# Performance work log

Measured on AMD Instinct MI355X. Metric: run time of the kernel, lower is better.

The kernel has to match this reference:

```python
import jax, jax.numpy as jnp
import numpy as np

D_MODEL = 1024
NUM_HEADS = 16
HEAD_DIM = D_MODEL // NUM_HEADS


def setup_inputs() -> dict:
    key = jax.random.key(0)
    ks = jax.random.split(key, 11)
    B, S, D = 2, 2048, D_MODEL
    scale = 1.0 / np.sqrt(D)
    inp = {
        "q": jax.random.normal(ks[0], (B, S, D), dtype=jnp.float32),
        "k": jax.random.normal(ks[1], (B, S, D), dtype=jnp.float32),
        "v": jax.random.normal(ks[2], (B, S, D), dtype=jnp.float32),
        # torch nn.Linear weights are [out, in]; y = x @ W.T + b
        "Wq": jax.random.normal(ks[3], (D, D), dtype=jnp.float32) * scale,
        "bq": jnp.zeros((D,), dtype=jnp.float32),
        "Wk": jax.random.normal(ks[4], (D, D), dtype=jnp.float32) * scale,
        "bk": jnp.zeros((D,), dtype=jnp.float32),
        "Wv": jax.random.normal(ks[5], (D, D), dtype=jnp.float32) * scale,
        "bv": jnp.zeros((D,), dtype=jnp.float32),
        "Wo": jax.random.normal(ks[6], (D, D), dtype=jnp.float32) * scale,
        "bo": jnp.zeros((D,), dtype=jnp.float32),
    }
    return inp


def _split_heads(x):
    B, S, D = x.shape
    return x.reshape(B, S, NUM_HEADS, HEAD_DIM).transpose(0, 2, 1, 3)  # [B,H,S,hd]


def reference(q, k, v, Wq, bq, Wk, bk, Wv, bv, Wo, bo):
    B, S, D = q.shape
    qh = _split_heads(q @ Wq.T + bq)
    kh = _split_heads(k @ Wk.T + bk)
    vh = _split_heads(v @ Wv.T + bv)
    # scores: [B,H,S,S], causal mask, softmax
    scores = jnp.einsum("bhqd,bhkd->bhqk", qh, kh) / jnp.sqrt(
        jnp.asarray(HEAD_DIM, dtype=qh.dtype))
    causal = jnp.tril(jnp.ones((S, S), dtype=bool))
    scores = jnp.where(causal[None, None], scores, -jnp.inf)
    attn = jax.nn.softmax(scores, axis=-1)
    out = jnp.einsum("bhqk,bhkd->bhqd", attn, vh)  # [B,H,S,hd]
    out = out.transpose(0, 2, 1, 3).reshape(B, S, D)
    return out @ Wo.T + bo
```

## Files before the change

kernel.cpp:

```cpp
#include <hip/hip_runtime.h>
#include <hip/hip_bf16.h>
#include <cstdint>
#include <cstddef>

typedef __bf16 bf16;
typedef __bf16 bf16x2 __attribute__((ext_vector_type(2)));
typedef __bf16 bf16x4 __attribute__((ext_vector_type(4)));
typedef __bf16 bf16x8 __attribute__((ext_vector_type(8)));
typedef float f32x4 __attribute__((ext_vector_type(4)));
typedef float f32x16 __attribute__((ext_vector_type(16)));
typedef unsigned int u32x4 __attribute__((ext_vector_type(4)));

#define S_LEN 2048
#define DM 1024
#define NH 16
#define HD 64
#define NQKV (4096 * 1024)
#define NW (1024 * 1024)
#define QK_SCALE 0.18033688011112042f

__device__ __forceinline__ void gload_lds16(const bf16* g, bf16* l) {
  __builtin_amdgcn_global_load_lds(
      (const __attribute__((address_space(1))) void*)g,
      (__attribute__((address_space(3))) void*)l, 16, 0, 0);
}

__device__ __forceinline__ unsigned packbf(float lo, float hi) {
  bf16x2 t;
  t[0] = (bf16)lo;
  t[1] = (bf16)hi;
  return __builtin_bit_cast(unsigned, t);
}

__device__ __forceinline__ void pl32swap(unsigned& a, unsigned& b) {
#if __has_builtin(__builtin_amdgcn_permlane32_swap)
  auto r = __builtin_amdgcn_permlane32_swap((int)a, (int)b, false, false);
  a = (unsigned)r[0];
  b = (unsigned)r[1];
#else
  asm volatile("v_permlane32_swap_b32 %0, %1" : "+v"(a), "+v"(b));
#endif
}

__global__ __launch_bounds__(256) void cvt_all(
    const float* __restrict__ q, const float* __restrict__ k, const float* __restrict__ v,
    const float* __restrict__ Wq, const float* __restrict__ Wk, const float* __restrict__ Wv,
    const float* __restrict__ Wo, bf16* __restrict__ out) {
  const size_t i = ((size_t)blockIdx.x * 256 + threadIdx.x) * 8;
  const float* src;
  size_t off;
  if (i < (size_t)NQKV) { src = q; off = i; }
  else if (i < 2ull * NQKV) { src = k; off = i - NQKV; }
  else if (i < 3ull * NQKV) { src = v; off = i - 2ull * NQKV; }
  else {
    const size_t j = i - 3ull * NQKV;
    if (j < (size_t)NW) { src = Wq; off = j; }
    else if (j < 2ull * NW) { src = Wk; off = j - NW; }
    else if (j < 3ull * NW) { src = Wv; off = j - 2ull * NW; }
    else { src = Wo; off = j - 3ull * NW; }
  }
  const float4 a = *(const float4*)(src + off);
  const float4 b = *(const float4*)(src + off + 4);
  bf16x8 o;
  o[0] = (bf16)a.x; o[1] = (bf16)a.y; o[2] = (bf16)a.z; o[3] = (bf16)a.w;
  o[4] = (bf16)b.x; o[5] = (bf16)b.y; o[6] = (bf16)b.z; o[7] = (bf16)b.w;
  *(bf16x8*)(out + i) = o;
}

template <int MODE>
__global__ __launch_bounds__(256, 2) void gemm_bt(
    const bf16* __restrict__ A, const bf16* __restrict__ W,
    const float* __restrict__ bias0, const float* __restrict__ bias1,
    const float* __restrict__ bias2, void* __restrict__ Out,
    int M, int N, int K, float scale) {
  __shared__ __align__(16) bf16 sm[2 * 128 * 64];
  bf16* Asl = sm;
  bf16* Bsl = sm + 128 * 64;
  const int tid = threadIdx.x;
  const int lane = tid & 63, w = tid >> 6;
  const int wr = w >> 1, wc = w & 1;
  const int r16 = lane & 15, grp = lane >> 4;

  int flat = blockIdx.y * gridDim.x + blockIdx.x;
  const int cpx = (gridDim.x * gridDim.y) >> 3;
  flat = (flat & 7) * cpx + (flat >> 3);
  const int m0 = (flat / gridDim.x) * 128;
  const int n0 = (flat % gridDim.x) * 128;

  const int seg = n0 >> 10;
  const bf16* Ab = (MODE == 3) ? A + (size_t)seg * NQKV : A;

  f32x4 acc[4][4] = {};

  const int nk = K >> 6;
  for (int t = 0; t < nk; ++t) {
    const int k0 = t << 6;
    __syncthreads();
#pragma unroll
    for (int j = 0; j < 4; ++j) {
      const int lin = j * 256 + tid;
      const int rr = lin >> 3;
      const int cc = (lin & 7) * 8;
      gload_lds16(&Ab[(size_t)(m0 + rr) * K + k0 + cc], &Asl[lin * 8]);
      gload_lds16(&W[(size_t)(n0 + rr) * K + k0 + cc], &Bsl[lin * 8]);
    }
    __syncthreads();
#pragma unroll
    for (int kk = 0; kk < 2; ++kk) {
      bf16x8 af[4], bfr[4];
#pragma unroll
      for (int m = 0; m < 4; ++m)
        af[m] = *(const bf16x8*)&Asl[(wr * 64 + m * 16 + r16) * 64 + kk * 32 + grp * 8];
#pragma unroll
      for (int n = 0; n < 4; ++n)
        bfr[n] = *(const bf16x8*)&Bsl[(wc * 64 + n * 16 + r16) * 64 + kk * 32 + grp * 8];
#pragma unroll
      for (int m = 0; m < 4; ++m)
#pragma unroll
        for (int n = 0; n < 4; ++n)
          acc[m][n] = __builtin_amdgcn_mfma_f32_16x16x32_bf16(af[m], bfr[n], acc[m][n], 0, 0, 0);
    }
  }

  const float* bp = (MODE == 3) ? (seg == 0 ? bias0 : (seg == 1 ? bias1 : bias2)) : bias0;
  const float sc = (MODE == 3) ? (seg == 0 ? scale : 1.0f) : scale;

  if (MODE == 3 && seg == 2) {
    __syncthreads();
    bf16* T = sm + w * (32 * 76);
    const int b = (m0 + wr * 64) >> 11;
    const int srow0 = (m0 + wr * 64) & 2047;
    bf16* base2 = (bf16*)Out + 2 * (size_t)NQKV;
#pragma unroll
    for (int p = 0; p < 2; ++p) {
#pragma unroll
      for (int nn = 0; nn < 2; ++nn) {
        const int n = 2 * p + nn;
#pragma unroll
        for (int mq = 0; mq < 4; ++mq)
#pragma unroll
          for (int r = 0; r < 4; ++r) {
            const int d_l = nn * 16 + r16;
            const int s_l = mq * 16 + grp * 4 + r;
            const int cs = (n0 + wc * 64 + n * 16 + r16) & 1023;
            T[d_l * 76 + s_l] = (bf16)(acc[mq][n][r] + bp[cs]);
          }
      }
      __syncthreads();
#pragma unroll
      for (int j = 0; j < 4; ++j) {
        const int d_l = j * 8 + (lane >> 3);
        const int scnk = lane & 7;
        const uint2 lo = *(const uint2*)&T[d_l * 76 + scnk * 8];
        const uint2 hi = *(const uint2*)&T[d_l * 76 + scnk * 8 + 4];
        const int cs = (n0 + wc * 64 + p * 32 + d_l) & 1023;
        const int hh = cs >> 6, dd = cs & 63;
        bf16* dst = base2 + ((size_t)(b * NH + hh) * HD + dd) * S_LEN + srow0 + scnk * 8;
        uint4 val; val.x = lo.x; val.y = lo.y; val.z = hi.x; val.w = hi.y;
        *(uint4*)dst = val;
      }
      __syncthreads();
    }
    return;
  }

#pragma unroll
  for (int m = 0; m < 4; ++m) {
#pragma unroll
    for (int n = 0; n < 4; ++n) {
#pragma unroll
      for (int r = 0; r < 4; ++r) {
        const int row = m0 + wr * 64 + m * 16 + grp * 4 + r;
        const int col = n0 + wc * 64 + n * 16 + r16;
        const int cs = col & 1023;
        const float v = (acc[m][n][r] + bp[cs]) * sc;
        if (MODE == 3) {
          const int b = row >> 11, s = row & 2047, h = cs >> 6, d = cs & 63;
          bf16* base = (bf16*)Out + (size_t)seg * NQKV;
          base[((size_t)(b * NH + h) * S_LEN + s) * HD + d] = (bf16)v;
        } else {
          ((float*)Out)[(size_t)row * N + col] = v;
        }
      }
    }
  }
}

__global__ __launch_bounds__(256, 2) void attn_fwd6(
    const bf16* __restrict__ Qh, const bf16* __restrict__ Kh,
    const bf16* __restrict__ Vt, bf16* __restrict__ AO) {
  __shared__ __align__(16) bf16 Kl[3][64 * 64];
  __shared__ __align__(16) bf16 Vl[3][64 * 64];

  const int tid = threadIdx.x;
  const int lane = tid & 63, w = tid >> 6;
  const int q31 = lane & 31, h = lane >> 5;

  const int bid = blockIdx.x;
  const int xcd = bid & 7;
  const int within = bid >> 3;
  const int bh = xcd * 4 + (within >> 4);
  const int cc = (within < 32) ? 15 - (within & 15) : (within & 15);
  const int q0 = cc * 128;
  const int nt = 2 * cc + 2;
  const int q0w = q0 + 32 * w;
  const int nt_w = (q0w >> 6) + 1;
  const int qg = q0w + q31;

  const bf16* Qb = Qh + (size_t)bh * S_LEN * HD;
  const bf16* Kb = Kh + (size_t)bh * S_LEN * HD;
  const bf16* Vb = Vt + (size_t)bh * HD * S_LEN;

  int stK[2], stV[2], stL[2];
#pragma unroll
  for (int i = 0; i < 2; ++i) {
    const int lin = i * 256 + tid;
    const int row = lin >> 3;
    const int colb = (lin & 7) * 16;
    const int scol = colb ^ ((row & 7) << 4);
    stK[i] = row * HD + (scol >> 1);
    stV[i] = row * S_LEN + (scol >> 1);
    stL[i] = lin * 8;
  }

  bf16x8 qf[4];
#pragma unroll
  for (int ks = 0; ks < 4; ++ks)
    qf[ks] = *(const bf16x8*)&Qb[(size_t)qg * HD + ks * 16 + 8 * h];

  f32x16 accO[2] = {};
  float m = -1e30f, l = 0.f;
  const int swz = (q31 & 7) << 4;

#pragma unroll
  for (int i = 0; i < 2; ++i) {
    gload_lds16(&Kb[stK[i]], &Kl[0][stL[i]]);
    gload_lds16(&Vb[stV[i]], &Vl[0][stL[i]]);
  }
  if (nt > 1) {
#pragma unroll
    for (int i = 0; i < 2; ++i) {
      gload_lds16(&Kb[(size_t)64 * HD + stK[i]], &Kl[1][stL[i]]);
      gload_lds16(&Vb[64 + stV[i]], &Vl[1][stL[i]]);
    }
  }

  int cur = 0;
  for (int kt = 0; kt < nt; ++kt) {
    if (kt + 1 < nt) asm volatile("s_waitcnt vmcnt(4)" ::: "memory");
    else             asm volatile("s_waitcnt vmcnt(0)" ::: "memory");
    __builtin_amdgcn_s_barrier();

    if (kt + 2 < nt) {
      int nxt = cur + 2; if (nxt >= 3) nxt -= 3;
      const int kn = (kt + 2) << 6;
      bf16* kd = Kl[nxt];
      bf16* vd = Vl[nxt];
#pragma unroll
      for (int i = 0; i < 2; ++i) {
        gload_lds16(&Kb[(size_t)kn * HD + stK[i]], &kd[stL[i]]);
        gload_lds16(&Vb[kn + stV[i]], &vd[stL[i]]);
      }
    }

    if (kt < nt_w) {
      const int k0 = kt << 6;
      const bf16* KlC = Kl[cur];
      const bf16* VlC = Vl[cur];
      const bool diag = (kt == nt_w - 1);
      const bool skip1 = diag && (k0 + 32 > q0w + 31);

      bf16x8 kf[8];
#pragma unroll
      for (int ks = 0; ks < 4; ++ks) {
        const int c = (32 * ks + 16 * h) ^ swz;
        kf[ks] = *(const bf16x8*)((const char*)KlC + q31 * 128 + c);
      }
      if (!skip1) {
#pragma unroll
        for (int ks = 0; ks < 4; ++ks) {
          const int c = (32 * ks + 16 * h) ^ swz;
          kf[4 + ks] = *(const bf16x8*)((const char*)KlC + (32 + q31) * 128 + c);
        }
      }

      f32x16 p0 = {}, p1 = {};
      __builtin_amdgcn_s_setprio(1);
#pragma unroll
      for (int ks = 0; ks < 4; ++ks)
        p0 = __builtin_amdgcn_mfma_f32_32x32x16_bf16(kf[ks], qf[ks], p0, 0, 0, 0);
      __builtin_amdgcn_s_setprio(0);
      if (!skip1) {
        __builtin_amdgcn_s_setprio(1);
#pragma unroll
        for (int ks = 0; ks < 4; ++ks)
          p1 = __builtin_amdgcn_mfma_f32_32x32x16_bf16(kf[4 + ks], qf[ks], p1, 0, 0, 0);
        __builtin_amdgcn_s_setprio(0);
      } else {
#pragma unroll
        for (int r = 0; r < 16; ++r) p1[r] = -1e30f;
      }

      bf16x8 vf01[4];
#pragma unroll
      for (int ks = 0; ks < 2; ++ks)
#pragma unroll
        for (int db = 0; db < 2; ++db) {
          const int c = (32 * ks + 16 * h) ^ swz;
          vf01[ks * 2 + db] =
              *(const bf16x8*)((const char*)VlC + (db * 32 + q31) * 128 + c);
        }

      if (diag) {
#pragma unroll
        for (int r = 0; r < 16; ++r) {
          const int key = k0 + (r & 3) + 8 * (r >> 2) + 4 * h;
          if (key > qg) p0[r] = -1e30f;
          if (!skip1 && key + 32 > qg) p1[r] = -1e30f;
        }
      }
      float t[16];
#pragma unroll
      for (int r = 0; r < 16; ++r) t[r] = fmaxf(p0[r], p1[r]);
#pragma unroll
      for (int s = 8; s >= 1; s >>= 1)
#pragma unroll
        for (int r = 0; r < s; ++r) t[r] = fmaxf(t[r], t[r + s]);
      const float pmax = fmaxf(t[0], __shfl_xor(t[0], 32));
      if (!__all(pmax - m <= 8.0f)) {
        const float mn = fmaxf(m, pmax);
        const float alpha = exp2f(m - mn);
        m = mn;
        l *= alpha;
#pragma unroll
        for (int r = 0; r < 16; ++r) { accO[0][r] *= alpha; accO[1][r] *= alpha; }
      }
      float smv[16];
#pragma unroll
      for (int r = 0; r < 16; ++r) {
        p0[r] = exp2f(p0[r] - m);
        p1[r] = exp2f(p1[r] - m);
        smv[r] = p0[r] + p1[r];
      }
#pragma unroll
      for (int s = 8; s >= 1; s >>= 1)
#pragma unroll
        for (int r = 0; r < s; ++r) smv[r] += smv[r + s];
      l += smv[0] + __shfl_xor(smv[0], 32);

      unsigned pw[4][4];
#define PACK_HALF(P, o0, o1)                                                   \
  {                                                                            \
    unsigned wv[8];                                                            \
    _Pragma("unroll") for (int mm = 0; mm < 8; ++mm)                           \
        wv[mm] = packbf(P[2 * mm], P[2 * mm + 1]);                             \
    pl32swap(wv[0], wv[2]);                                                    \
    pl32swap(wv[1], wv[3]);                                                    \
    pl32swap(wv[4], wv[6]);                                                    \
    pl32swap(wv[5], wv[7]);                                                    \
    pw[o0][0] = wv[0]; pw[o0][1] = wv[1]; pw[o0][2] = wv[2]; pw[o0][3] = wv[3];\
    pw[o1][0] = wv[4]; pw[o1][1] = wv[5]; pw[o1][2] = wv[6]; pw[o1][3] = wv[7];\
  }
      PACK_HALF(p0, 0, 1)
      if (!skip1) PACK_HALF(p1, 2, 3)
#undef PACK_HALF

      bf16x8 vf23[4];
      if (!skip1) {
#pragma unroll
        for (int ks = 2; ks < 4; ++ks)
#pragma unroll
          for (int db = 0; db < 2; ++db) {
            const int c = (32 * ks + 16 * h) ^ swz;
            vf23[(ks - 2) * 2 + db] =
                *(const bf16x8*)((const char*)VlC + (db * 32 + q31) * 128 + c);
          }
      }

#define PV_STEP(ks, vfa)                                                       \
  {                                                                            \
    u32x4 pu = {pw[ks][0], pw[ks][1], pw[ks][2], pw[ks][3]};                   \
    const bf16x8 pf_ = __builtin_bit_cast(bf16x8, pu);                         \
    accO[0] = __builtin_amdgcn_mfma_f32_32x32x16_bf16(vfa[(ks & 1) * 2 + 0],   \
                                                      pf_, accO[0], 0, 0, 0);  \
    accO[1] = __builtin_amdgcn_mfma_f32_32x32x16_bf16(vfa[(ks & 1) * 2 + 1],   \
                                                      pf_, accO[1], 0, 0, 0);  \
  }
      __builtin_amdgcn_s_setprio(1);
      PV_STEP(0, vf01)
      PV_STEP(1, vf01)
      __builtin_amdgcn_s_setprio(0);
      if (!skip1) {
        __builtin_amdgcn_s_setprio(1);
        PV_STEP(2, vf23)
        PV_STEP(3, vf23)
        __builtin_amdgcn_s_setprio(0);
      }
#undef PV_STEP
    }

    ++cur; if (cur == 3) cur = 0;
  }

  const float ro = 1.0f / l;
  const int b = bh >> 4, hh = bh & 15;
  bf16* orow = AO + ((size_t)(b * S_LEN + qg)) * DM + hh * HD;
#pragma unroll
  for (int db = 0; db < 2; ++db) {
#pragma unroll
    for (int mm = 0; mm < 4; ++mm) {
      bf16x4 ov;
#pragma unroll
      for (int t = 0; t < 4; ++t) ov[t] = (bf16)(accO[db][4 * mm + t] * ro);
      *(bf16x4*)&orow[db * 32 + 8 * mm + 4 * h] = ov;
    }
  }
}

extern "C" void kernel_launch(void* const* d_in, const int* in_sizes, int n_in,
                              void* d_out, int out_size, void* d_ws, size_t ws_size,
                              hipStream_t stream) {
  const float* q  = (const float*)d_in[0];
  const float* k  = (const float*)d_in[1];
  const float* v  = (const float*)d_in[2];
  const float* Wq = (const float*)d_in[3];
  const float* bq = (const float*)d_in[4];
  const float* Wk = (const float*)d_in[5];
  const float* bk = (const float*)d_in[6];
  const float* Wv = (const float*)d_in[7];
  const float* bv = (const float*)d_in[8];
  const float* Wo = (const float*)d_in[9];
  const float* bo = (const float*)d_in[10];

  const int NTOK = 2 * S_LEN;

  bf16* qb  = (bf16*)d_ws;
  bf16* Wqb = qb + 3 * (size_t)NQKV;
  bf16* Wob = Wqb + 3 * (size_t)NW;
  bf16* Qh  = Wqb + 4 * (size_t)NW;
  bf16* Kh  = Qh + (size_t)NQKV;
  bf16* Vt  = Kh + (size_t)NQKV;
  bf16* AO  = Vt + (size_t)NQKV;

  const int cvt_blocks = (3 * NQKV + 4 * NW) / 8 / 256;
  cvt_all<<<cvt_blocks, 256, 0, stream>>>(q, k, v, Wq, Wk, Wv, Wo, qb);

  gemm_bt<3><<<dim3(3 * DM / 128, NTOK / 128), 256, 0, stream>>>(
      qb, Wqb, bq, bk, bv, Qh, NTOK, 3 * DM, DM, QK_SCALE);

  attn_fwd6<<<dim3(512), 256, 0, stream>>>(Qh, Kh, Vt, AO);

  gemm_bt<2><<<dim3(DM / 128, NTOK / 128), 256, 0, stream>>>(
      AO, Wob, bo, bo, bo, d_out, NTOK, DM, DM, 1.0f);
}
```

Measured before the change: 133.2 us.

## Restructure attention blocks to pair low and high causal query chunks per wave

Each block now has 2 waves instead of 4. Each wave processes two 32-row query chunks, one near the start and one near the end of the sequence, so every block does the same amount of causal work. K/V tiles staged in LDS are reused across both chunks, which raises data reuse per load, and the per-block load imbalance of the old mapping goes away. The cost is more register pressure from holding two sets of accumulators and Q fragments, occupancy set to 1 block per CU at 128 threads, and fewer waves to hide latency.

After: 153.3 us. +15.1%, slower.

```diff
diff --git a/kernel.cpp b/kernel.cpp
--- a/kernel.cpp
+++ b/kernel.cpp
@@ -186,7 +186,7 @@
   }
 }
 
-__global__ __launch_bounds__(256, 2) void attn_fwd6(
+__global__ __launch_bounds__(128, 1) void attn_fwd7(
     const bf16* __restrict__ Qh, const bf16* __restrict__ Kh,
     const bf16* __restrict__ Vt, bf16* __restrict__ AO) {
   __shared__ __align__(16) bf16 Kl[3][64 * 64];
@@ -199,22 +199,24 @@
   const int bid = blockIdx.x;
   const int xcd = bid & 7;
   const int within = bid >> 3;
-  const int bh = xcd * 4 + (within >> 4);
-  const int cc = (within < 32) ? 15 - (within & 15) : (within & 15);
-  const int q0 = cc * 128;
-  const int nt = 2 * cc + 2;
-  const int q0w = q0 + 32 * w;
-  const int nt_w = (q0w >> 6) + 1;
-  const int qg = q0w + q31;
+  const int j = within >> 2;
+  const int bh = xcd * 4 + (within & 3);
+
+  const int cL = 2 * j + w;
+  const int qL = cL << 5;
+  const int qH = (63 - cL) << 5;
+  const int ntL = j + 1;
+  const int nt = 32 - j;
+  const int qgL = qL + q31, qgH = qH + q31;
 
   const bf16* Qb = Qh + (size_t)bh * S_LEN * HD;
   const bf16* Kb = Kh + (size_t)bh * S_LEN * HD;
   const bf16* Vb = Vt + (size_t)bh * HD * S_LEN;
 
-  int stK[2], stV[2], stL[2];
-#pragma unroll
-  for (int i = 0; i < 2; ++i) {
-    const int lin = i * 256 + tid;
+  int stK[4], stV[4], stL[4];
+#pragma unroll
+  for (int i = 0; i < 4; ++i) {
+    const int lin = i * 128 + tid;
     const int row = lin >> 3;
     const int colb = (lin & 7) * 16;
     const int scol = colb ^ ((row & 7) << 4);
@@ -223,133 +225,33 @@
     stL[i] = lin * 8;
   }
 
-  bf16x8 qf[4];
-#pragma unroll
-  for (int ks = 0; ks < 4; ++ks)
-    qf[ks] = *(const bf16x8*)&Qb[(size_t)qg * HD + ks * 16 + 8 * h];
-
-  f32x16 accO[2] = {};
-  float m = -1e30f, l = 0.f;
+#define STAGE(t, buf)                                                          \
+  {                                                                            \
+    const bf16* kb_ = Kb + (size_t)(t) * 64 * HD;                              \
+    const bf16* vb_ = Vb + (t) * 64;                                           \
+    bf16* kd_ = &Kl[buf][0];                                                   \
+    bf16* vd_ = &Vl[buf][0];                                                   \
+    _Pragma("unroll") for (int i = 0; i < 4; ++i) {                            \
+      gload_lds16(kb_ + stK[i], kd_ + stL[i]);                                 \
+      gload_lds16(vb_ + stV[i], vd_ + stL[i]);                                 \
+    }                                                                          \
+  }
+
+  bf16x8 qfL[4], qfH[4];
+#pragma unroll
+  for (int ks = 0; ks < 4; ++ks) {
+    qfL[ks] = *(const bf16x8*)&Qb[(size_t)qgL * HD + ks * 16 + 8 * h];
+    qfH[ks] = *(const bf16x8*)&Qb[(size_t)qgH * HD + ks * 16 + 8 * h];
+  }
+
+  f32x16 accL0 = {}, accL1 = {}, accH0 = {}, accH1 = {};
+  float mL = -1e30f, lL = 0.f, mH = -1e30f, lH = 0.f;
   const int swz = (q31 & 7) << 4;
 
-#pragma unroll
-  for (int i = 0; i < 2; ++i) {
-    gload_lds16(&Kb[stK[i]], &Kl[0][stL[i]]);
-    gload_lds16(&Vb[stV[i]], &Vl[0][stL[i]]);
-  }
-  if (nt > 1) {
-#pragma unroll
-    for (int i = 0; i < 2; ++i) {
-      gload_lds16(&Kb[(size_t)64 * HD + stK[i]], &Kl[1][stL[i]]);
-      gload_lds16(&Vb[64 + stV[i]], &Vl[1][stL[i]]);
-    }
-  }
-
-  int cur = 0;
-  for (int kt = 0; kt < nt; ++kt) {
-    if (kt + 1 < nt) asm volatile("s_waitcnt vmcnt(4)" ::: "memory");
-    else             asm volatile("s_waitcnt vmcnt(0)" ::: "memory");
-    __builtin_amdgcn_s_barrier();
-
-    if (kt + 2 < nt) {
-      int nxt = cur + 2; if (nxt >= 3) nxt -= 3;
-      const int kn = (kt + 2) << 6;
-      bf16* kd = Kl[nxt];
-      bf16* vd = Vl[nxt];
-#pragma unroll
-      for (int i = 0; i < 2; ++i) {
-        gload_lds16(&Kb[(size_t)kn * HD + stK[i]], &kd[stL[i]]);
-        gload_lds16(&Vb[kn + stV[i]], &vd[stL[i]]);
-      }
-    }
-
-    if (kt < nt_w) {
-      const int k0 = kt << 6;
-      const bf16* KlC = Kl[cur];
-      const bf16* VlC = Vl[cur];
-      const bool diag = (kt == nt_w - 1);
-      const bool skip1 = diag && (k0 + 32 > q0w + 31);
-
-      bf16x8 kf[8];
-#pragma unroll
-      for (int ks = 0; ks < 4; ++ks) {
-        const int c = (32 * ks + 16 * h) ^ swz;
-        kf[ks] = *(const bf16x8*)((const char*)KlC + q31 * 128 + c);
-      }
-      if (!skip1) {
-#pragma unroll
-        for (int ks = 0; ks < 4; ++ks) {
-          const int c = (32 * ks + 16 * h) ^ swz;
-          kf[4 + ks] = *(const bf16x8*)((const char*)KlC + (32 + q31) * 128 + c);
-        }
-      }
-
-      f32x16 p0 = {}, p1 = {};
-      __builtin_amdgcn_s_setprio(1);
-#pragma unroll
-      for (int ks = 0; ks < 4; ++ks)
-        p0 = __builtin_amdgcn_mfma_f32_32x32x16_bf16(kf[ks], qf[ks], p0, 0, 0, 0);
-      __builtin_amdgcn_s_setprio(0);
-      if (!skip1) {
-        __builtin_amdgcn_s_setprio(1);
-#pragma unroll
-        for (int ks = 0; ks < 4; ++ks)
-          p1 = __builtin_amdgcn_mfma_f32_32x32x16_bf16(kf[4 + ks], qf[ks], p1, 0, 0, 0);
-        __builtin_amdgcn_s_setprio(0);
-      } else {
-#pragma unroll
-        for (int r = 0; r < 16; ++r) p1[r] = -1e30f;
-      }
-
-      bf16x8 vf01[4];
-#pragma unroll
-      for (int ks = 0; ks < 2; ++ks)
-#pragma unroll
-        for (int db = 0; db < 2; ++db) {
-          const int c = (32 * ks + 16 * h) ^ swz;
-          vf01[ks * 2 + db] =
-              *(const bf16x8*)((const char*)VlC + (db * 32 + q31) * 128 + c);
-        }
-
-      if (diag) {
-#pragma unroll
-        for (int r = 0; r < 16; ++r) {
-          const int key = k0 + (r & 3) + 8 * (r >> 2) + 4 * h;
-          if (key > qg) p0[r] = -1e30f;
-          if (!skip1 && key + 32 > qg) p1[r] = -1e30f;
-        }
-      }
-      float t[16];
-#pragma unroll
-      for (int r = 0; r < 16; ++r) t[r] = fmaxf(p0[r], p1[r]);
-#pragma unroll
-      for (int s = 8; s >= 1; s >>= 1)
-#pragma unroll
-        for (int r = 0; r < s; ++r) t[r] = fmaxf(t[r], t[r + s]);
-      const float pmax = fmaxf(t[0], __shfl_xor(t[0], 32));
-      if (!__all(pmax - m <= 8.0f)) {
-        const float mn = fmaxf(m, pmax);
-        const float alpha = exp2f(m - mn);
-        m = mn;
-        l *= alpha;
-#pragma unroll
-        for (int r = 0; r < 16; ++r) { accO[0][r] *= alpha; accO[1][r] *= alpha; }
-      }
-      float smv[16];
-#pragma unroll
-      for (int r = 0; r < 16; ++r) {
-        p0[r] = exp2f(p0[r] - m);
-        p1[r] = exp2f(p1[r] - m);
-        smv[r] = p0[r] + p1[r];
-      }
-#pragma unroll
-      for (int s = 8; s >= 1; s >>= 1)
-#pragma unroll
-        for (int r = 0; r < s; ++r) smv[r] += smv[r + s];
-      l += smv[0] + __shfl_xor(smv[0], 32);
-
-      unsigned pw[4][4];
-#define PACK_HALF(P, o0, o1)                                                   \
+  STAGE(0, 0)
+  STAGE(1, 1)
+
+#define PACK_HALF(P, PW, o0, o1)                                               \
   {                                                                            \
     unsigned wv[8];                                                            \
     _Pragma("unroll") for (int mm = 0; mm < 8; ++mm)                           \
@@ -358,63 +260,190 @@
     pl32swap(wv[1], wv[3]);                                                    \
     pl32swap(wv[4], wv[6]);                                                    \
     pl32swap(wv[5], wv[7]);                                                    \
-    pw[o0][0] = wv[0]; pw[o0][1] = wv[1]; pw[o0][2] = wv[2]; pw[o0][3] = wv[3];\
-    pw[o1][0] = wv[4]; pw[o1][1] = wv[5]; pw[o1][2] = wv[6]; pw[o1][3] = wv[7];\
-  }
-      PACK_HALF(p0, 0, 1)
-      if (!skip1) PACK_HALF(p1, 2, 3)
+    PW[o0][0] = wv[0]; PW[o0][1] = wv[1]; PW[o0][2] = wv[2]; PW[o0][3] = wv[3];\
+    PW[o1][0] = wv[4]; PW[o1][1] = wv[5]; PW[o1][2] = wv[6]; PW[o1][3] = wv[7];\
+  }
+
+#define SOFTMAX_PACK(P0, P1, A0, A1, M, L, PW, SKIP1)                          \
+  {                                                                            \
+    float t_[16];                                                              \
+    _Pragma("unroll") for (int r = 0; r < 16; ++r)                             \
+        t_[r] = fmaxf(P0[r], P1[r]);                                           \
+    _Pragma("unroll") for (int s = 8; s >= 1; s >>= 1)                         \
+      _Pragma("unroll") for (int r = 0; r < s; ++r)                            \
+          t_[r] = fmaxf(t_[r], t_[r + s]);                                     \
+    const float pmax_ = fmaxf(t_[0], __shfl_xor(t_[0], 32));                   \
+    if (!__all(pmax_ - M <= 8.0f)) {                                           \
+      const float mn_ = fmaxf(M, pmax_);                                       \
+      const float al_ = exp2f(M - mn_);                                        \
+      M = mn_;                                                                 \
+      L *= al_;                                                                \
+      _Pragma("unroll") for (int r = 0; r < 16; ++r) {                         \
+        A0[r] *= al_;                                                          \
+        A1[r] *= al_;                                                          \
+      }                                                                        \
+    }                                                                          \
+    float sv_[16];                                                             \
+    _Pragma("unroll") for (int r = 0; r < 16; ++r) {                           \
+      P0[r] = exp2f(P0[r] - M);                                                \
+      P1[r] = exp2f(P1[r] - M);                                                \
+      sv_[r] = P0[r] + P1[r];                                                  \
+    }                                                                          \
+    _Pragma("unroll") for (int s = 8; s >= 1; s >>= 1)                         \
+      _Pragma("unroll") for (int r = 0; r < s; ++r) sv_[r] += sv_[r + s];      \
+    L += sv_[0] + __shfl_xor(sv_[0], 32);                                      \
+    PACK_HALF(P0, PW, 0, 1)                                                    \
+    if (!(SKIP1)) PACK_HALF(P1, PW, 2, 3)                                      \
+  }
+
+#define PV_STEP(PW, ks, A0, A1)                                                \
+  {                                                                            \
+    u32x4 pu = {PW[ks][0], PW[ks][1], PW[ks][2], PW[ks][3]};                   \
+    const bf16x8 pf_ = __builtin_bit_cast(bf16x8, pu);                         \
+    A0 = __builtin_amdgcn_mfma_f32_32x32x16_bf16(vf[(ks) * 2 + 0], pf_, A0,    \
+                                                 0, 0, 0);                     \
+    A1 = __builtin_amdgcn_mfma_f32_32x32x16_bf16(vf[(ks) * 2 + 1], pf_, A1,    \
+                                                 0, 0, 0);                     \
+  }
+
+  int cur = 0;
+  for (int kt = 0; kt < nt; ++kt) {
+    if (kt + 1 < nt) asm volatile("s_waitcnt vmcnt(8)" ::: "memory");
+    else             asm volatile("s_waitcnt vmcnt(0)" ::: "memory");
+    __builtin_amdgcn_s_barrier();
+
+    if (kt + 2 < nt) {
+      int nxt = cur + 2; if (nxt >= 3) nxt -= 3;
+      STAGE(kt + 2, nxt)
+    }
+
+    const int k0 = kt << 6;
+    const bf16* KlC = &Kl[cur][0];
+    const bf16* VlC = &Vl[cur][0];
+
+    const bool liveL = kt < ntL;
+    const bool skipL = (kt == ntL - 1) && (w == 0);
+    const bool skipH = (kt == nt - 1) && (w == 1);
+
+    bf16x8 kf[8];
+#pragma unroll
+    for (int ks = 0; ks < 4; ++ks) {
+      const int c = (32 * ks + 16 * h) ^ swz;
+      kf[ks]     = *(const bf16x8*)((const char*)KlC + q31 * 128 + c);
+      kf[4 + ks] = *(const bf16x8*)((const char*)KlC + (32 + q31) * 128 + c);
+    }
+
+    f32x16 pL0 = {}, pL1 = {}, pH0 = {}, pH1 = {};
+    __builtin_amdgcn_s_setprio(1);
+    if (liveL) {
+#pragma unroll
+      for (int ks = 0; ks < 4; ++ks)
+        pL0 = __builtin_amdgcn_mfma_f32_32x32x16_bf16(kf[ks], qfL[ks], pL0, 0, 0, 0);
+      if (!skipL) {
+#pragma unroll
+        for (int ks = 0; ks < 4; ++ks)
+          pL1 = __builtin_amdgcn_mfma_f32_32x32x16_bf16(kf[4 + ks], qfL[ks], pL1, 0, 0, 0);
+      }
+    }
+#pragma unroll
+    for (int ks = 0; ks < 4; ++ks)
+      pH0 = __builtin_amdgcn_mfma_f32_32x32x16_bf16(kf[ks], qfH[ks], pH0, 0, 0, 0);
+    if (!skipH) {
+#pragma unroll
+      for (int ks = 0; ks < 4; ++ks)
+        pH1 = __builtin_amdgcn_mfma_f32_32x32x16_bf16(kf[4 + ks], qfH[ks], pH1, 0, 0, 0);
+    }
+    __builtin_amdgcn_s_setprio(0);
+
+    bf16x8 vf[8];
+#pragma unroll
+    for (int ks = 0; ks < 4; ++ks)
+#pragma unroll
+      for (int db = 0; db < 2; ++db) {
+        const int c = (32 * ks + 16 * h) ^ swz;
+        vf[ks * 2 + db] =
+            *(const bf16x8*)((const char*)VlC + (db * 32 + q31) * 128 + c);
+      }
+
+    if (liveL && kt == ntL - 1) {
+      if (skipL) {
+#pragma unroll
+        for (int r = 0; r < 16; ++r) {
+          const int key = k0 + (r & 3) + 8 * (r >> 2) + 4 * h;
+          if (key > qgL) pL0[r] = -1e30f;
+          pL1[r] = -1e30f;
+        }
+      } else {
+#pragma unroll
+        for (int r = 0; r < 16; ++r) {
+          const int key = k0 + 32 + (r & 3) + 8 * (r >> 2) + 4 * h;
+          if (key > qgL) pL1[r] = -1e30f;
+        }
+      }
+    }
+    if (kt == nt - 1) {
+      if (skipH) {
+#pragma unroll
+        for (int r = 0; r < 16; ++r) {
+          const int key = k0 + (r & 3) + 8 * (r >> 2) + 4 * h;
+          if (key > qgH) pH0[r] = -1e30f;
+          pH1[r] = -1e30f;
+        }
+      } else {
+#pragma unroll
+        for (int r = 0; r < 16; ++r) {
+          const int key = k0 + 32 + (r & 3) + 8 * (r >> 2) + 4 * h;
+          if (key > qgH) pH1[r] = -1e30f;
+        }
+      }
+    }
+
+    unsigned pwL[4][4], pwH[4][4];
+    if (liveL) SOFTMAX_PACK(pL0, pL1, accL0, accL1, mL, lL, pwL, skipL)
+    SOFTMAX_PACK(pH0, pH1, accH0, accH1, mH, lH, pwH, skipH)
+
+    __builtin_amdgcn_s_setprio(1);
+    if (liveL) {
+      PV_STEP(pwL, 0, accL0, accL1)
+      PV_STEP(pwL, 1, accL0, accL1)
+      if (!skipL) {
+        PV_STEP(pwL, 2, accL0, accL1)
+        PV_STEP(pwL, 3, accL0, accL1)
+      }
+    }
+    PV_STEP(pwH, 0, accH0, accH1)
+    PV_STEP(pwH, 1, accH0, accH1)
+    if (!skipH) {
+      PV_STEP(pwH, 2, accH0, accH1)
+      PV_STEP(pwH, 3, accH0, accH1)
+    }
+    __builtin_amdgcn_s_setprio(0);
+
+    ++cur; if (cur == 3) cur = 0;
+  }
+
+  const int b = bh >> 4, hh = bh & 15;
+#define STORE_CHAIN(A0, A1, LVAL, QG)                                          \
+  {                                                                            \
+    const float ro_ = 1.0f / (LVAL);                                           \
+    bf16* orow_ = AO + ((size_t)(b * S_LEN + (QG))) * DM + hh * HD;            \
+    _Pragma("unroll") for (int mm = 0; mm < 4; ++mm) {                         \
+      bf16x4 ov0, ov1;                                                         \
+      _Pragma("unroll") for (int t2 = 0; t2 < 4; ++t2) {                       \
+        ov0[t2] = (bf16)(A0[4 * mm + t2] * ro_);                               \
+        ov1[t2] = (bf16)(A1[4 * mm + t2] * ro_);                               \
+      }                                                                        \
+      *(bf16x4*)&orow_[8 * mm + 4 * h] = ov0;                                  \
+      *(bf16x4*)&orow_[32 + 8 * mm + 4 * h] = ov1;                             \
+    }                                                                          \
+  }
+  STORE_CHAIN(accL0, accL1, lL, qgL)
+  STORE_CHAIN(accH0, accH1, lH, qgH)
+#undef STORE_CHAIN
+#undef PV_STEP
+#undef SOFTMAX_PACK
 #undef PACK_HALF
-
-      bf16x8 vf23[4];
-      if (!skip1) {
-#pragma unroll
-        for (int ks = 2; ks < 4; ++ks)
-#pragma unroll
-          for (int db = 0; db < 2; ++db) {
-            const int c = (32 * ks + 16 * h) ^ swz;
-            vf23[(ks - 2) * 2 + db] =
-                *(const bf16x8*)((const char*)VlC + (db * 32 + q31) * 128 + c);
-          }
-      }
-
-#define PV_STEP(ks, vfa)                                                       \
-  {                                                                            \
-    u32x4 pu = {pw[ks][0], pw[ks][1], pw[ks][2], pw[ks][3]};                   \
-    const bf16x8 pf_ = __builtin_bit_cast(bf16x8, pu);                         \
-    accO[0] = __builtin_amdgcn_mfma_f32_32x32x16_bf16(vfa[(ks & 1) * 2 + 0],   \
-                                                      pf_, accO[0], 0, 0, 0);  \
-    accO[1] = __builtin_amdgcn_mfma_f32_32x32x16_bf16(vfa[(ks & 1) * 2 + 1],   \
-                                                      pf_, accO[1], 0, 0, 0);  \
-  }
-      __builtin_amdgcn_s_setprio(1);
-      PV_STEP(0, vf01)
-      PV_STEP(1, vf01)
-      __builtin_amdgcn_s_setprio(0);
-      if (!skip1) {
-        __builtin_amdgcn_s_setprio(1);
-        PV_STEP(2, vf23)
-        PV_STEP(3, vf23)
-        __builtin_amdgcn_s_setprio(0);
-      }
-#undef PV_STEP
-    }
-
-    ++cur; if (cur == 3) cur = 0;
-  }
-
-  const float ro = 1.0f / l;
-  const int b = bh >> 4, hh = bh & 15;
-  bf16* orow = AO + ((size_t)(b * S_LEN + qg)) * DM + hh * HD;
-#pragma unroll
-  for (int db = 0; db < 2; ++db) {
-#pragma unroll
-    for (int mm = 0; mm < 4; ++mm) {
-      bf16x4 ov;
-#pragma unroll
-      for (int t = 0; t < 4; ++t) ov[t] = (bf16)(accO[db][4 * mm + t] * ro);
-      *(bf16x4*)&orow[db * 32 + 8 * mm + 4 * h] = ov;
-    }
-  }
+#undef STAGE
 }
 
 extern "C" void kernel_launch(void* const* d_in, const int* in_sizes, int n_in,
@@ -448,7 +477,7 @@
   gemm_bt<3><<<dim3(3 * DM / 128, NTOK / 128), 256, 0, stream>>>(
       qb, Wqb, bq, bk, bv, Qh, NTOK, 3 * DM, DM, QK_SCALE);
 
-  attn_fwd6<<<dim3(512), 256, 0, stream>>>(Qh, Kh, Vt, AO);
+  attn_fwd7<<<dim3(512), 128, 0, stream>>>(Qh, Kh, Vt, AO);
 
   gemm_bt<2><<<dim3(DM / 128, NTOK / 128), 256, 0, stream>>>(
       AO, Wob, bo, bo, bo, d_out, NTOK, DM, DM, 1.0f);
```

## Split attention keys across wave pairs and pair causal chunks per block

Applied to the files above, without the earlier changes.

Each block now handles two 64-query chunks (p and 31-p) so every block does the same amount of causal work. Within a chunk, four waves split into two query halves times two key halves: each wave computes one 32x32 score tile per key tile. Partial softmax states are merged through LDS at the end. This aims to even out the causal load across blocks and waves and to shorten per-wave dependency chains, at the cost of extra barriers, an LDS reduction, and smaller per-chunk tiles with their own pipeline prologue.

Measured after the change: 121.3 us. 8.9% less time.

```diff
diff --git a/kernel.cpp b/kernel.cpp
--- a/kernel.cpp
+++ b/kernel.cpp
@@ -186,7 +186,7 @@
   }
 }
 
-__global__ __launch_bounds__(256, 2) void attn_fwd6(
+__global__ __launch_bounds__(256, 2) void attn_fwd8(
     const bf16* __restrict__ Qh, const bf16* __restrict__ Kh,
     const bf16* __restrict__ Vt, bf16* __restrict__ AO) {
   __shared__ __align__(16) bf16 Kl[3][64 * 64];
@@ -195,17 +195,14 @@
   const int tid = threadIdx.x;
   const int lane = tid & 63, w = tid >> 6;
   const int q31 = lane & 31, h = lane >> 5;
+  const int qh = w >> 1, kh = w & 1;
+  const int koff = kh << 5;
 
   const int bid = blockIdx.x;
   const int xcd = bid & 7;
   const int within = bid >> 3;
-  const int bh = xcd * 4 + (within >> 4);
-  const int cc = (within < 32) ? 15 - (within & 15) : (within & 15);
-  const int q0 = cc * 128;
-  const int nt = 2 * cc + 2;
-  const int q0w = q0 + 32 * w;
-  const int nt_w = (q0w >> 6) + 1;
-  const int qg = q0w + q31;
+  const int bh = xcd * 4 + (within & 3);
+  const int p = within >> 2;
 
   const bf16* Qb = Qh + (size_t)bh * S_LEN * HD;
   const bf16* Kb = Kh + (size_t)bh * S_LEN * HD;
@@ -222,199 +219,170 @@
     stV[i] = row * S_LEN + (scol >> 1);
     stL[i] = lin * 8;
   }
-
-  bf16x8 qf[4];
-#pragma unroll
-  for (int ks = 0; ks < 4; ++ks)
-    qf[ks] = *(const bf16x8*)&Qb[(size_t)qg * HD + ks * 16 + 8 * h];
-
-  f32x16 accO[2] = {};
-  float m = -1e30f, l = 0.f;
   const int swz = (q31 & 7) << 4;
 
-#pragma unroll
-  for (int i = 0; i < 2; ++i) {
-    gload_lds16(&Kb[stK[i]], &Kl[0][stL[i]]);
-    gload_lds16(&Vb[stV[i]], &Vl[0][stL[i]]);
-  }
-  if (nt > 1) {
-#pragma unroll
-    for (int i = 0; i < 2; ++i) {
-      gload_lds16(&Kb[(size_t)64 * HD + stK[i]], &Kl[1][stL[i]]);
-      gload_lds16(&Vb[64 + stV[i]], &Vl[1][stL[i]]);
-    }
-  }
-
-  int cur = 0;
-  for (int kt = 0; kt < nt; ++kt) {
-    if (kt + 1 < nt) asm volatile("s_waitcnt vmcnt(4)" ::: "memory");
-    else             asm volatile("s_waitcnt vmcnt(0)" ::: "memory");
-    __builtin_amdgcn_s_barrier();
-
-    if (kt + 2 < nt) {
-      int nxt = cur + 2; if (nxt >= 3) nxt -= 3;
-      const int kn = (kt + 2) << 6;
-      bf16* kd = Kl[nxt];
-      bf16* vd = Vl[nxt];
-#pragma unroll
-      for (int i = 0; i < 2; ++i) {
-        gload_lds16(&Kb[(size_t)kn * HD + stK[i]], &kd[stL[i]]);
-        gload_lds16(&Vb[kn + stV[i]], &vd[stL[i]]);
-      }
-    }
-
-    if (kt < nt_w) {
-      const int k0 = kt << 6;
-      const bf16* KlC = Kl[cur];
-      const bf16* VlC = Vl[cur];
-      const bool diag = (kt == nt_w - 1);
-      const bool skip1 = diag && (k0 + 32 > q0w + 31);
-
-      bf16x8 kf[8];
-#pragma unroll
-      for (int ks = 0; ks < 4; ++ks) {
-        const int c = (32 * ks + 16 * h) ^ swz;
-        kf[ks] = *(const bf16x8*)((const char*)KlC + q31 * 128 + c);
-      }
-      if (!skip1) {
+#define STAGE(t, buf)                                                          \
+  {                                                                            \
+    const bf16* kb_ = Kb + (size_t)(t) * 64 * HD;                              \
+    const bf16* vb_ = Vb + (t) * 64;                                           \
+    _Pragma("unroll") for (int i = 0; i < 2; ++i) {                            \
+      gload_lds16(kb_ + stK[i], &Kl[buf][stL[i]]);                             \
+      gload_lds16(vb_ + stV[i], &Vl[buf][stL[i]]);                             \
+    }                                                                          \
+  }
+
+  auto run_chunk = [&](const int q0, const int nt) {
+    const int q0w = q0 + (qh << 5);
+    const int qg = q0w + q31;
+    const int nt_w = (w == 1) ? nt - 1 : nt;
+    const bool maskw = (w == 0) || (w == 3);
+
+    bf16x8 qf[4];
+#pragma unroll
+    for (int ks = 0; ks < 4; ++ks)
+      qf[ks] = *(const bf16x8*)&Qb[(size_t)qg * HD + ks * 16 + 8 * h];
+
+    f32x16 acc0 = {}, acc1 = {};
+    float m = -1e30f, l = 0.f;
+
+    STAGE(0, 0)
+    STAGE(1, 1)
+
+    int cur = 0;
+    for (int kt = 0; kt < nt; ++kt) {
+      if (kt + 1 < nt) asm volatile("s_waitcnt vmcnt(4)" ::: "memory");
+      else             asm volatile("s_waitcnt vmcnt(0)" ::: "memory");
+      __builtin_amdgcn_s_barrier();
+
+      if (kt + 2 < nt) {
+        int nxt = cur + 2; if (nxt >= 3) nxt -= 3;
+        STAGE(kt + 2, nxt)
+      }
+
+      if (kt < nt_w) {
+        const bf16* KlC = &Kl[cur][0];
+        const bf16* VlC = &Vl[cur][0];
+
+        bf16x8 kf[4];
 #pragma unroll
         for (int ks = 0; ks < 4; ++ks) {
           const int c = (32 * ks + 16 * h) ^ swz;
-          kf[4 + ks] = *(const bf16x8*)((const char*)KlC + (32 + q31) * 128 + c);
-        }
-      }
-
-      f32x16 p0 = {}, p1 = {};
-      __builtin_amdgcn_s_setprio(1);
-#pragma unroll
-      for (int ks = 0; ks < 4; ++ks)
-        p0 = __builtin_amdgcn_mfma_f32_32x32x16_bf16(kf[ks], qf[ks], p0, 0, 0, 0);
-      __builtin_amdgcn_s_setprio(0);
-      if (!skip1) {
+          kf[ks] = *(const bf16x8*)((const char*)KlC + (koff + q31) * 128 + c);
+        }
+
+        f32x16 p0 = {};
         __builtin_amdgcn_s_setprio(1);
 #pragma unroll
         for (int ks = 0; ks < 4; ++ks)
-          p1 = __builtin_amdgcn_mfma_f32_32x32x16_bf16(kf[4 + ks], qf[ks], p1, 0, 0, 0);
+          p0 = __builtin_amdgcn_mfma_f32_32x32x16_bf16(kf[ks], qf[ks], p0, 0, 0, 0);
         __builtin_amdgcn_s_setprio(0);
-      } else {
-#pragma unroll
-        for (int r = 0; r < 16; ++r) p1[r] = -1e30f;
-      }
-
-      bf16x8 vf01[4];
-#pragma unroll
-      for (int ks = 0; ks < 2; ++ks)
-#pragma unroll
-        for (int db = 0; db < 2; ++db) {
-          const int c = (32 * ks + 16 * h) ^ swz;
-          vf01[ks * 2 + db] =
-              *(const bf16x8*)((const char*)VlC + (db * 32 + q31) * 128 + c);
-        }
-
-      if (diag) {
-#pragma unroll
-        for (int r = 0; r < 16; ++r) {
-          const int key = k0 + (r & 3) + 8 * (r >> 2) + 4 * h;
-          if (key > qg) p0[r] = -1e30f;
-          if (!skip1 && key + 32 > qg) p1[r] = -1e30f;
-        }
-      }
-      float t[16];
-#pragma unroll
-      for (int r = 0; r < 16; ++r) t[r] = fmaxf(p0[r], p1[r]);
-#pragma unroll
-      for (int s = 8; s >= 1; s >>= 1)
-#pragma unroll
-        for (int r = 0; r < s; ++r) t[r] = fmaxf(t[r], t[r + s]);
-      const float pmax = fmaxf(t[0], __shfl_xor(t[0], 32));
-      if (!__all(pmax - m <= 8.0f)) {
-        const float mn = fmaxf(m, pmax);
-        const float alpha = exp2f(m - mn);
-        m = mn;
-        l *= alpha;
-#pragma unroll
-        for (int r = 0; r < 16; ++r) { accO[0][r] *= alpha; accO[1][r] *= alpha; }
-      }
-      float smv[16];
-#pragma unroll
-      for (int r = 0; r < 16; ++r) {
-        p0[r] = exp2f(p0[r] - m);
-        p1[r] = exp2f(p1[r] - m);
-        smv[r] = p0[r] + p1[r];
-      }
-#pragma unroll
-      for (int s = 8; s >= 1; s >>= 1)
-#pragma unroll
-        for (int r = 0; r < s; ++r) smv[r] += smv[r + s];
-      l += smv[0] + __shfl_xor(smv[0], 32);
-
-      unsigned pw[4][4];
-#define PACK_HALF(P, o0, o1)                                                   \
-  {                                                                            \
-    unsigned wv[8];                                                            \
-    _Pragma("unroll") for (int mm = 0; mm < 8; ++mm)                           \
-        wv[mm] = packbf(P[2 * mm], P[2 * mm + 1]);                             \
-    pl32swap(wv[0], wv[2]);                                                    \
-    pl32swap(wv[1], wv[3]);                                                    \
-    pl32swap(wv[4], wv[6]);                                                    \
-    pl32swap(wv[5], wv[7]);                                                    \
-    pw[o0][0] = wv[0]; pw[o0][1] = wv[1]; pw[o0][2] = wv[2]; pw[o0][3] = wv[3];\
-    pw[o1][0] = wv[4]; pw[o1][1] = wv[5]; pw[o1][2] = wv[6]; pw[o1][3] = wv[7];\
-  }
-      PACK_HALF(p0, 0, 1)
-      if (!skip1) PACK_HALF(p1, 2, 3)
-#undef PACK_HALF
-
-      bf16x8 vf23[4];
-      if (!skip1) {
-#pragma unroll
-        for (int ks = 2; ks < 4; ++ks)
+
+        bf16x8 vf[4];
+#pragma unroll
+        for (int ks = 0; ks < 2; ++ks)
 #pragma unroll
           for (int db = 0; db < 2; ++db) {
-            const int c = (32 * ks + 16 * h) ^ swz;
-            vf23[(ks - 2) * 2 + db] =
+            const int c = (64 * kh + 32 * ks + 16 * h) ^ swz;
+            vf[ks * 2 + db] =
                 *(const bf16x8*)((const char*)VlC + (db * 32 + q31) * 128 + c);
           }
-      }
-
-#define PV_STEP(ks, vfa)                                                       \
-  {                                                                            \
-    u32x4 pu = {pw[ks][0], pw[ks][1], pw[ks][2], pw[ks][3]};                   \
-    const bf16x8 pf_ = __builtin_bit_cast(bf16x8, pu);                         \
-    accO[0] = __builtin_amdgcn_mfma_f32_32x32x16_bf16(vfa[(ks & 1) * 2 + 0],   \
-                                                      pf_, accO[0], 0, 0, 0);  \
-    accO[1] = __builtin_amdgcn_mfma_f32_32x32x16_bf16(vfa[(ks & 1) * 2 + 1],   \
-                                                      pf_, accO[1], 0, 0, 0);  \
-  }
-      __builtin_amdgcn_s_setprio(1);
-      PV_STEP(0, vf01)
-      PV_STEP(1, vf01)
-      __builtin_amdgcn_s_setprio(0);
-      if (!skip1) {
+
+        if (maskw && kt == nt - 1) {
+#pragma unroll
+          for (int r = 0; r < 16; ++r) {
+            const int key = (kt << 6) + koff + (r & 3) + 8 * (r >> 2) + 4 * h;
+            if (key > qg) p0[r] = -1e30f;
+          }
+        }
+        float t_[16];
+#pragma unroll
+        for (int r = 0; r < 16; ++r) t_[r] = p0[r];
+#pragma unroll
+        for (int s = 8; s >= 1; s >>= 1)
+#pragma unroll
+          for (int r = 0; r < s; ++r) t_[r] = fmaxf(t_[r], t_[r + s]);
+        const float pmax = fmaxf(t_[0], __shfl_xor(t_[0], 32));
+        if (!__all(pmax - m <= 8.0f)) {
+          const float mn = fmaxf(m, pmax);
+          const float al = exp2f(m - mn);
+          m = mn;
+          l *= al;
+#pragma unroll
+          for (int r = 0; r < 16; ++r) { acc0[r] *= al; acc1[r] *= al; }
+        }
+        float sv[16];
+#pragma unroll
+        for (int r = 0; r < 16; ++r) {
+          p0[r] = exp2f(p0[r] - m);
+          sv[r] = p0[r];
+        }
+#pragma unroll
+        for (int s = 8; s >= 1; s >>= 1)
+#pragma unroll
+          for (int r = 0; r < s; ++r) sv[r] += sv[r + s];
+        l += sv[0] + __shfl_xor(sv[0], 32);
+
+        unsigned wv[8];
+#pragma unroll
+        for (int mm = 0; mm < 8; ++mm)
+          wv[mm] = packbf(p0[2 * mm], p0[2 * mm + 1]);
+        pl32swap(wv[0], wv[2]);
+        pl32swap(wv[1], wv[3]);
+        pl32swap(wv[4], wv[6]);
+        pl32swap(wv[5], wv[7]);
+
         __builtin_amdgcn_s_setprio(1);
-        PV_STEP(2, vf23)
-        PV_STEP(3, vf23)
+        {
+          u32x4 pu0 = {wv[0], wv[1], wv[2], wv[3]};
+          const bf16x8 pf0 = __builtin_bit_cast(bf16x8, pu0);
+          acc0 = __builtin_amdgcn_mfma_f32_32x32x16_bf16(vf[0], pf0, acc0, 0, 0, 0);
+          acc1 = __builtin_amdgcn_mfma_f32_32x32x16_bf16(vf[1], pf0, acc1, 0, 0, 0);
+          u32x4 pu1 = {wv[4], wv[5], wv[6], wv[7]};
+          const bf16x8 pf1 = __builtin_bit_cast(bf16x8, pu1);
+          acc0 = __builtin_amdgcn_mfma_f32_32x32x16_bf16(vf[2], pf1, acc0, 0, 0, 0);
+          acc1 = __builtin_amdgcn_mfma_f32_32x32x16_bf16(vf[3], pf1, acc1, 0, 0, 0);
+        }
         __builtin_amdgcn_s_setprio(0);
       }
-#undef PV_STEP
-    }
-
-    ++cur; if (cur == 3) cur = 0;
-  }
-
-  const float ro = 1.0f / l;
-  const int b = bh >> 4, hh = bh & 15;
-  bf16* orow = AO + ((size_t)(b * S_LEN + qg)) * DM + hh * HD;
-#pragma unroll
-  for (int db = 0; db < 2; ++db) {
-#pragma unroll
-    for (int mm = 0; mm < 4; ++mm) {
-      bf16x4 ov;
-#pragma unroll
-      for (int t = 0; t < 4; ++t) ov[t] = (bf16)(accO[db][4 * mm + t] * ro);
-      *(bf16x4*)&orow[db * 32 + 8 * mm + 4 * h] = ov;
-    }
-  }
+
+      ++cur; if (cur == 3) cur = 0;
+    }
+
+    float* scr = (float*)&Kl[0][0];
+    float* s = scr + (size_t)qh * (64 * 34) + lane * 34;
+    __syncthreads();
+    if (kh) {
+#pragma unroll
+      for (int r = 0; r < 16; ++r) { s[r] = acc0[r]; s[16 + r] = acc1[r]; }
+      s[32] = m;
+      s[33] = l;
+    }
+    __syncthreads();
+    if (!kh) {
+      const float m1 = s[32], l1 = s[33];
+      const float mn = fmaxf(m, m1);
+      const float a0 = exp2f(m - mn), a1 = exp2f(m1 - mn);
+      const float linv = 1.0f / (a0 * l + a1 * l1);
+      const int b = bh >> 4, hh = bh & 15;
+      bf16* orow = AO + ((size_t)(b * S_LEN + qg)) * DM + hh * HD;
+#pragma unroll
+      for (int mm = 0; mm < 4; ++mm) {
+        bf16x4 ov0, ov1;
+#pragma unroll
+        for (int t2 = 0; t2 < 4; ++t2) {
+          ov0[t2] = (bf16)((a0 * acc0[4 * mm + t2] + a1 * s[4 * mm + t2]) * linv);
+          ov1[t2] = (bf16)((a0 * acc1[4 * mm + t2] + a1 * s[16 + 4 * mm + t2]) * linv);
+        }
+        *(bf16x4*)&orow[8 * mm + 4 * h] = ov0;
+        *(bf16x4*)&orow[32 + 8 * mm + 4 * h] = ov1;
+      }
+    }
+    __syncthreads();
+  };
+
+  run_chunk(p << 6, p + 1);
+  run_chunk((31 - p) << 6, 32 - p);
+#undef STAGE
 }
 
 extern "C" void kernel_launch(void* const* d_in, const int* in_sizes, int n_in,
@@ -448,7 +416,7 @@
   gemm_bt<3><<<dim3(3 * DM / 128, NTOK / 128), 256, 0, stream>>>(
       qb, Wqb, bq, bk, bv, Qh, NTOK, 3 * DM, DM, QK_SCALE);
 
-  attn_fwd6<<<dim3(512), 256, 0, stream>>>(Qh, Kh, Vt, AO);
+  attn_fwd8<<<dim3(512), 256, 0, stream>>>(Qh, Kh, Vt, AO);
 
   gemm_bt<2><<<dim3(DM / 128, NTOK / 128), 256, 0, stream>>>(
       AO, Wob, bo, bo, bo, d_out, NTOK, DM, DM, 1.0f);
```
